# Kernel tuning notes

Measured on AMD Instinct MI355X. Metric: run time of the kernel, lower is better.

The kernel has to match this reference:

```python
import jax, jax.numpy as jnp
import numpy as np

B, S, D, H = 8, 2048, 768, 12

def setup_inputs() -> dict:
    key = jax.random.key(0)
    kx, km, kk, kq, kv = jax.random.split(key, 5)
    return {
        "x": jax.random.normal(kx, (B, S, D), dtype=jnp.float32),
        "mask": jax.random.randint(km, (B, 1, S), 0, 2, dtype=jnp.int32),
        "key_weight": jax.random.normal(kk, (D, H), dtype=jnp.float32),
        "query_weight": jax.random.normal(kq, (D, H), dtype=jnp.float32),
        "value_weight": jax.random.normal(kv, (D, H), dtype=jnp.float32),
    }

def reference(x, mask, key_weight, query_weight, value_weight):
    scale = 1.0 / (key_weight.shape[-1] ** 0.5)
    k = jnp.einsum('bsd,dh->bsh', x, key_weight)
    q = jnp.einsum('bsd,dh->bsh', x, query_weight)
    v = jnp.einsum('bsd,dh->bsh', x, value_weight)
    # scores: (B, S, T) — full score matrix as in the original
    scores = jnp.einsum('bsh,bth->bst', q, k) * scale
    scores = jnp.where(mask == 0, -jnp.inf, scores)
    attn = jax.nn.softmax(scores, axis=-1)
    return jnp.einsum('bst,bth->bsh', attn, v)
```

## Files before the change

### kernel.cpp

```cpp
#include <hip/hip_runtime.h>
#include <math.h>

#define QSCALE (0.2886751345948129f * 1.4426950408889634f)

#if __has_builtin(__builtin_amdgcn_exp2f)
#define EXP2F(x) __builtin_amdgcn_exp2f(x)
#else
#define EXP2F(x) exp2f(x)
#endif

typedef __attribute__((ext_vector_type(8))) _Float16 half8;
typedef __attribute__((ext_vector_type(4))) _Float16 half4_t;
typedef __attribute__((ext_vector_type(4))) float floatx4;

#define MFMA32F16(a, b, c) __builtin_amdgcn_mfma_f32_16x16x32_f16((a), (b), (c), 0, 0, 0)
#define MFMA16F16(a, b, c) __builtin_amdgcn_mfma_f32_16x16x16f16((a), (b), (c), 0, 0, 0)

static __device__ inline float bperm(float v, int addr_bytes) {
    return __int_as_float(__builtin_amdgcn_ds_bpermute(addr_bytes, __float_as_int(v)));
}

__global__ __launch_bounds__(256)
void wswz(const float* __restrict__ Wq, const float* __restrict__ Wk,
          const float* __restrict__ Wv, _Float16* __restrict__ wfh,
          _Float16* __restrict__ wfl)
{
    int t = blockIdx.x * 256 + threadIdx.x;
    if (t >= 4608) return;
    int lane = t & 63;
    int nt   = (t >> 6) % 3;
    int ks   = t / 192;
    const float* W = (nt == 0) ? Wq : (nt == 1) ? Wk : Wv;
    const float scale = (nt == 0) ? QSCALE : 1.0f;
    int col = lane & 15;
    int q8  = lane >> 4;
    half8 hi, lo;
    #pragma unroll
    for (int j = 0; j < 8; ++j) {
        int dim = ks * 32 + q8 * 8 + j;
        float f = (col < 12) ? W[dim * 12 + col] * scale : 0.0f;
        _Float16 h = (_Float16)f;
        hi[j] = h;
        lo[j] = (_Float16)(f - (float)h);
    }
    size_t off = ((size_t)(ks * 3 + nt) * 64 + lane) * 8;
    *(half8*)(wfh + off) = hi;
    *(half8*)(wfl + off) = lo;
}

__global__ __launch_bounds__(256)
void mask_scan(const int* __restrict__ mask, int* __restrict__ dst,
               int* __restrict__ nvalid)
{
    __shared__ int cnt[256];
    const int b = blockIdx.x;
    const int t = threadIdx.x;
    const int* mb = mask + b * 2048;
    int local[8]; int c = 0;
    #pragma unroll
    for (int i = 0; i < 8; ++i) { local[i] = (mb[t * 8 + i] != 0); c += local[i]; }
    cnt[t] = c;
    __syncthreads();
    for (int off = 1; off < 256; off <<= 1) {
        int u = cnt[t];
        int add = (t >= off) ? cnt[t - off] : 0;
        __syncthreads();
        cnt[t] = u + add;
        __syncthreads();
    }
    int run = (t == 0) ? 0 : cnt[t - 1];
    int* db = dst + b * 2048;
    #pragma unroll
    for (int i = 0; i < 8; ++i) { db[t * 8 + i] = local[i] ? run : -1; run += local[i]; }
    if (t == 255) nvalid[b] = cnt[255];
}

__global__ __launch_bounds__(256)
void zero_frag(float4* __restrict__ p, int n)
{
    int i = blockIdx.x * 256 + threadIdx.x;
    float4 z = make_float4(0.f, 0.f, 0.f, 0.f);
    if (i < n) p[i] = z;
}

__global__ __launch_bounds__(256, 2)
void qkv_mfma(const float* __restrict__ x, const _Float16* __restrict__ wfh,
              const _Float16* __restrict__ wfl, const int* __restrict__ dst,
              _Float16* __restrict__ qfh, _Float16* __restrict__ qfl,
              _Float16* __restrict__ kfh, _Float16* __restrict__ kfl,
              _Float16* __restrict__ vtf)
{
    __shared__ float xs[12352];
    const int tid  = threadIdx.x;
    const int lane = tid & 63;
    const int w    = tid >> 6;
    const int g    = blockIdx.x;
    const int rowbase = g * 16;

    {
        const int r  = tid >> 4;
        const int c0 = (tid & 15) * 4;
        const float* xr = x + (size_t)(rowbase + r) * 768 + c0;
        float* xd = xs + r * 772 + c0;
        #pragma unroll
        for (int i = 0; i < 12; ++i) {
            float4 v = *(const float4*)(xr + i * 64);
            *(float4*)(xd + i * 64) = v;
        }
    }
    __syncthreads();

    floatx4 acc0 = {0.f, 0.f, 0.f, 0.f};
    floatx4 acc1 = acc0, acc2 = acc0;
    const int m15 = lane & 15;
    const int q8  = lane >> 4;
    const float* xsrc = xs + m15 * 772 + q8 * 8;
    const half8* WH = (const half8*)wfh;
    const half8* WL = (const half8*)wfl;

    #pragma unroll
    for (int s6 = 0; s6 < 6; ++s6) {
        const int ks = w * 6 + s6;
        float xv[8];
        *(float4*)(xv)     = *(const float4*)(xsrc + ks * 32);
        *(float4*)(xv + 4) = *(const float4*)(xsrc + ks * 32 + 4);
        half8 ah, al;
        #pragma unroll
        for (int j = 0; j < 8; ++j) {
            _Float16 h = (_Float16)xv[j];
            ah[j] = h;
            al[j] = (_Float16)(xv[j] - (float)h);
        }
        half8 b0h = WH[(ks * 3 + 0) * 64 + lane];
        half8 b1h = WH[(ks * 3 + 1) * 64 + lane];
        half8 b2h = WH[(ks * 3 + 2) * 64 + lane];
        half8 b0l = WL[(ks * 3 + 0) * 64 + lane];
        half8 b1l = WL[(ks * 3 + 1) * 64 + lane];
        half8 b2l = WL[(ks * 3 + 2) * 64 + lane];
        acc0 = MFMA32F16(ah, b0h, acc0);
        acc1 = MFMA32F16(ah, b1h, acc1);
        acc2 = MFMA32F16(ah, b2h, acc2);
        acc0 = MFMA32F16(al, b0h, acc0);
        acc1 = MFMA32F16(al, b1h, acc1);
        acc2 = MFMA32F16(al, b2h, acc2);
        acc0 = MFMA32F16(ah, b0l, acc0);
        acc1 = MFMA32F16(ah, b1l, acc1);
        acc2 = MFMA32F16(ah, b2l, acc2);
    }

    __syncthreads();
    float* cbuf = xs;
    *(floatx4*)(cbuf + ((w * 3 + 0) * 64 + lane) * 4) = acc0;
    *(floatx4*)(cbuf + ((w * 3 + 1) * 64 + lane) * 4) = acc1;
    *(floatx4*)(cbuf + ((w * 3 + 2) * 64 + lane) * 4) = acc2;
    __syncthreads();
    if (w < 3) {
        floatx4 t0 = *(const floatx4*)(cbuf + ((0 * 3 + w) * 64 + lane) * 4);
        floatx4 t1 = *(const floatx4*)(cbuf + ((1 * 3 + w) * 64 + lane) * 4);
        floatx4 t2 = *(const floatx4*)(cbuf + ((2 * 3 + w) * 64 + lane) * 4);
        floatx4 t3 = *(const floatx4*)(cbuf + ((3 * 3 + w) * 64 + lane) * 4);
        floatx4 tot = t0 + t1 + t2 + t3;
        const int col = m15;
        const int r0  = q8 * 4;
        #pragma unroll
        for (int r = 0; r < 4; ++r) {
            const int row = rowbase + r0 + r;
            const float val = tot[r];
            if (w == 0) {
                if (col < 12) {
                    size_t off = ((size_t)g * 64 + (col >> 3) * 16 + (r0 + r)) * 8 + (col & 7);
                    _Float16 h = (_Float16)val;
                    qfh[off] = h;
                    qfl[off] = (_Float16)(val - (float)h);
                }
            } else {
                const int d = dst[row];
                if (d >= 0) {
                    const int bb = row >> 11;
                    if (w == 1) {
                        if (col < 12) {
                            size_t off = (((size_t)(bb * 128 + (d >> 4))) * 64
                                          + (col >> 3) * 16 + (d & 15)) * 8 + (col & 7);
                            _Float16 h = (_Float16)val;
                            kfh[off] = h;
                            kfl[off] = (_Float16)(val - (float)h);
                        }
                    } else {
                        if (col < 12) {
                            size_t off = (((size_t)(bb * 128 + (d >> 4))) * 64
                                          + ((d & 15) >> 2) * 16 + col) * 4 + (d & 3);
                            vtf[off] = (_Float16)val;
                        } else if (col == 12) {
                            size_t off = (((size_t)(bb * 128 + (d >> 4))) * 64
                                          + ((d & 15) >> 2) * 16 + 12) * 4 + (d & 3);
                            vtf[off] = (_Float16)1.0f;
                        }
                    }
                }
            }
        }
    }
}

__global__ __launch_bounds__(256)
void attn(const _Float16* __restrict__ qfh, const _Float16* __restrict__ qfl,
          const _Float16* __restrict__ kfh, const _Float16* __restrict__ kfl,
          const _Float16* __restrict__ vtf, const int* __restrict__ nvalid,
          float* __restrict__ out)
{
    __shared__ float cm[256];
    __shared__ __align__(16) floatx4 co[256];
    const int tid  = threadIdx.x;
    const int lane = tid & 63;
    const int w    = tid >> 6;
    const int g    = blockIdx.x;
    const int bb   = g >> 7;
    const int m15  = lane & 15;

    const half8 qh = *(const half8*)(qfh + ((size_t)g * 64 + lane) * 8);
    const half8 ql = *(const half8*)(qfl + ((size_t)g * 64 + lane) * 8);

    const half8* KH = (const half8*)kfh + (size_t)bb * 128 * 64;
    const half8* KL = (const half8*)kfl + (size_t)bb * 128 * 64;
    const half4_t* VT = (const half4_t*)vtf + (size_t)bb * 128 * 64;

    const int nv = nvalid[bb];
    const int nt = (nv + 15) >> 4;
    const int a16 = (lane ^ 16) << 2;
    const int a32 = (lane ^ 32) << 2;

    float mrow = -INFINITY;
    floatx4 o = {0.f, 0.f, 0.f, 0.f};

    int t = w;
    half8 kh, kl;
    half4_t va;
    if (t < nt) {
        kh = KH[t * 64 + lane];
        kl = KL[t * 64 + lane];
        va = VT[t * 64 + lane];
    }
    for (; t < nt; t += 4) {
        half8 nkh, nkl; half4_t nva;
        if (t + 4 < nt) {
            nkh = KH[(t + 4) * 64 + lane];
            nkl = KL[(t + 4) * 64 + lane];
            nva = VT[(t + 4) * 64 + lane];
        }
        floatx4 s = {0.f, 0.f, 0.f, 0.f};
        s = MFMA32F16(kh, qh, s);
        s = MFMA32F16(kl, qh, s);
        s = MFMA32F16(kh, ql, s);
        float pm = fmaxf(fmaxf(s.x, s.y), fmaxf(s.z, s.w));
        pm = fmaxf(pm, bperm(pm, a16));
        pm = fmaxf(pm, bperm(pm, a32));
        float mnew = fmaxf(mrow, pm);
        float corr = EXP2F(mrow - mnew);
        o.x *= corr; o.y *= corr; o.z *= corr; o.w *= corr;
        half4_t pb;
        pb[0] = (_Float16)EXP2F(s.x - mnew);
        pb[1] = (_Float16)EXP2F(s.y - mnew);
        pb[2] = (_Float16)EXP2F(s.z - mnew);
        pb[3] = (_Float16)EXP2F(s.w - mnew);
        o = MFMA16F16(va, pb, o);
        mrow = mnew;
        kh = nkh; kl = nkl; va = nva;
    }

    cm[w * 64 + lane] = mrow;
    co[w * 64 + lane] = o;
    __syncthreads();
    float gm = -INFINITY;
    #pragma unroll
    for (int w2 = 0; w2 < 4; ++w2) gm = fmaxf(gm, cm[w2 * 64 + lane]);
    floatx4 O = {0.f, 0.f, 0.f, 0.f};
    #pragma unroll
    for (int w2 = 0; w2 < 4; ++w2) {
        float f = EXP2F(cm[w2 * 64 + lane] - gm);
        floatx4 ow = co[w2 * 64 + lane];
        O.x += ow.x * f; O.y += ow.y * f; O.z += ow.z * f; O.w += ow.w * f;
    }
    float L = bperm(O.x, (48 + m15) << 2);
    float inv = 1.0f / L;
    if (w == 0 && (lane >> 4) < 3) {
        float4 ov = make_float4(O.x * inv, O.y * inv, O.z * inv, O.w * inv);
        *(float4*)(out + ((size_t)g * 16 + m15) * 12 + (lane >> 4) * 4) = ov;
    }
}

extern "C" void kernel_launch(void* const* d_in, const int* in_sizes, int n_in,
                              void* d_out, int out_size, void* d_ws, size_t ws_size,
                              hipStream_t stream) {
    const float* x    = (const float*)d_in[0];
    const int*   mask = (const int*)  d_in[1];
    const float* Wk   = (const float*)d_in[2];
    const float* Wq   = (const float*)d_in[3];
    const float* Wv   = (const float*)d_in[4];
    float* out = (float*)d_out;

    char* base = (char*)d_ws;
    _Float16* qfh = (_Float16*)(base);
    _Float16* qfl = (_Float16*)(base + (1u << 20));
    _Float16* kfh = (_Float16*)(base + (2u << 20));
    _Float16* kfl = (_Float16*)(base + (3u << 20));
    _Float16* vtf = (_Float16*)(base + (4u << 20));
    _Float16* wfh = (_Float16*)(base + 4718592);
    _Float16* wfl = (_Float16*)(base + 4718592 + 73728);
    int* dst      = (int*)(base + 4866048);
    int* nvalid   = (int*)(base + 4866048 + 65536);

    const int zero_n = 4718592 / 16;
    wswz<<<18, 256, 0, stream>>>(Wq, Wk, Wv, wfh, wfl);
    mask_scan<<<8, 256, 0, stream>>>(mask, dst, nvalid);
    zero_frag<<<(zero_n + 255) / 256, 256, 0, stream>>>((float4*)base, zero_n);
    qkv_mfma<<<1024, 256, 0, stream>>>(x, wfh, wfl, dst, qfh, qfl, kfh, kfl, vtf);
    attn<<<1024, 256, 0, stream>>>(qfh, qfl, kfh, kfl, vtf, nvalid, out);
}
```

Measured before the change: 115.2 us.

## Fuse prep kernels, load x directly in QKV, and process two query tiles per attention block

Merges the weight swizzle, mask scan and fragment zeroing into one prep launch, and zeroes only the K/V fragment region. The QKV kernel reads x straight from global memory into registers instead of staging it in LDS, prefetches weight fragments with double buffering, and targets higher occupancy. The attention kernel handles two 16-row query tiles per block, so each K/V fragment load feeds two score/PV computations, and blocks are interleaved across batches. Register pressure rises in both kernels, and the reduced zeroing range assumes the Q buffers are fully overwritten.

```diff
diff --git a/kernel.cpp b/kernel.cpp
--- a/kernel.cpp
+++ b/kernel.cpp
@@ -21,135 +21,133 @@
 }
 
 __global__ __launch_bounds__(256)
-void wswz(const float* __restrict__ Wq, const float* __restrict__ Wk,
-          const float* __restrict__ Wv, _Float16* __restrict__ wfh,
-          _Float16* __restrict__ wfl)
+void prep(const float* __restrict__ Wq, const float* __restrict__ Wk,
+          const float* __restrict__ Wv, const int* __restrict__ mask,
+          _Float16* __restrict__ wfh, _Float16* __restrict__ wfl,
+          int* __restrict__ dst, int* __restrict__ nvalid,
+          float4* __restrict__ zbase)
 {
-    int t = blockIdx.x * 256 + threadIdx.x;
-    if (t >= 4608) return;
-    int lane = t & 63;
-    int nt   = (t >> 6) % 3;
-    int ks   = t / 192;
-    const float* W = (nt == 0) ? Wq : (nt == 1) ? Wk : Wv;
-    const float scale = (nt == 0) ? QSCALE : 1.0f;
-    int col = lane & 15;
-    int q8  = lane >> 4;
-    half8 hi, lo;
-    #pragma unroll
-    for (int j = 0; j < 8; ++j) {
-        int dim = ks * 32 + q8 * 8 + j;
-        float f = (col < 12) ? W[dim * 12 + col] * scale : 0.0f;
-        _Float16 h = (_Float16)f;
-        hi[j] = h;
-        lo[j] = (_Float16)(f - (float)h);
-    }
-    size_t off = ((size_t)(ks * 3 + nt) * 64 + lane) * 8;
-    *(half8*)(wfh + off) = hi;
-    *(half8*)(wfl + off) = lo;
-}
-
-__global__ __launch_bounds__(256)
-void mask_scan(const int* __restrict__ mask, int* __restrict__ dst,
-               int* __restrict__ nvalid)
-{
-    __shared__ int cnt[256];
     const int b = blockIdx.x;
-    const int t = threadIdx.x;
-    const int* mb = mask + b * 2048;
-    int local[8]; int c = 0;
-    #pragma unroll
-    for (int i = 0; i < 8; ++i) { local[i] = (mb[t * 8 + i] != 0); c += local[i]; }
-    cnt[t] = c;
-    __syncthreads();
-    for (int off = 1; off < 256; off <<= 1) {
-        int u = cnt[t];
-        int add = (t >= off) ? cnt[t - off] : 0;
+    const int tid = threadIdx.x;
+    if (b < 18) {
+        int t = b * 256 + tid;
+        if (t >= 4608) return;
+        int lane = t & 63;
+        int nt   = (t >> 6) % 3;
+        int ks   = t / 192;
+        const float* W = (nt == 0) ? Wq : (nt == 1) ? Wk : Wv;
+        const float scale = (nt == 0) ? QSCALE : 1.0f;
+        int col = lane & 15;
+        int q8  = lane >> 4;
+        half8 hi, lo;
+        #pragma unroll
+        for (int j = 0; j < 8; ++j) {
+            int dim = ks * 32 + q8 * 8 + j;
+            float f = (col < 12) ? W[dim * 12 + col] * scale : 0.0f;
+            _Float16 h = (_Float16)f;
+            hi[j] = h;
+            lo[j] = (_Float16)(f - (float)h);
+        }
+        size_t off = ((size_t)(ks * 3 + nt) * 64 + lane) * 8;
+        *(half8*)(wfh + off) = hi;
+        *(half8*)(wfl + off) = lo;
+    } else if (b < 26) {
+        __shared__ int cnt[256];
+        const int bb = b - 18;
+        const int* mb = mask + bb * 2048;
+        int local[8]; int c = 0;
+        #pragma unroll
+        for (int i = 0; i < 8; ++i) { local[i] = (mb[tid * 8 + i] != 0); c += local[i]; }
+        cnt[tid] = c;
         __syncthreads();
-        cnt[t] = u + add;
-        __syncthreads();
-    }
-    int run = (t == 0) ? 0 : cnt[t - 1];
-    int* db = dst + b * 2048;
-    #pragma unroll
-    for (int i = 0; i < 8; ++i) { db[t * 8 + i] = local[i] ? run : -1; run += local[i]; }
-    if (t == 255) nvalid[b] = cnt[255];
-}
-
-__global__ __launch_bounds__(256)
-void zero_frag(float4* __restrict__ p, int n)
-{
-    int i = blockIdx.x * 256 + threadIdx.x;
-    float4 z = make_float4(0.f, 0.f, 0.f, 0.f);
-    if (i < n) p[i] = z;
-}
-
-__global__ __launch_bounds__(256, 2)
+        for (int off = 1; off < 256; off <<= 1) {
+            int u = cnt[tid];
+            int add = (tid >= off) ? cnt[tid - off] : 0;
+            __syncthreads();
+            cnt[tid] = u + add;
+            __syncthreads();
+        }
+        int run = (tid == 0) ? 0 : cnt[tid - 1];
+        int* db = dst + bb * 2048;
+        #pragma unroll
+        for (int i = 0; i < 8; ++i) { db[tid * 8 + i] = local[i] ? run : -1; run += local[i]; }
+        if (tid == 255) nvalid[bb] = cnt[255];
+    } else {
+        const float4 z = make_float4(0.f, 0.f, 0.f, 0.f);
+        for (int i = (b - 26) * 256 + tid; i < 163840; i += 6 * 256) zbase[i] = z;
+    }
+}
+
+__global__ __launch_bounds__(256, 3)
 void qkv_mfma(const float* __restrict__ x, const _Float16* __restrict__ wfh,
               const _Float16* __restrict__ wfl, const int* __restrict__ dst,
               _Float16* __restrict__ qfh, _Float16* __restrict__ qfl,
               _Float16* __restrict__ kfh, _Float16* __restrict__ kfl,
               _Float16* __restrict__ vtf)
 {
-    __shared__ float xs[12352];
+    __shared__ __align__(16) float cbuf[3072];
     const int tid  = threadIdx.x;
     const int lane = tid & 63;
     const int w    = tid >> 6;
     const int g    = blockIdx.x;
     const int rowbase = g * 16;
-
-    {
-        const int r  = tid >> 4;
-        const int c0 = (tid & 15) * 4;
-        const float* xr = x + (size_t)(rowbase + r) * 768 + c0;
-        float* xd = xs + r * 772 + c0;
-        #pragma unroll
-        for (int i = 0; i < 12; ++i) {
-            float4 v = *(const float4*)(xr + i * 64);
-            *(float4*)(xd + i * 64) = v;
-        }
-    }
-    __syncthreads();
+    const int m15 = lane & 15;
+    const int q8  = lane >> 4;
+
+    const float* xbase = x + (size_t)(rowbase + m15) * 768 + q8 * 8;
+    const half8* WH = (const half8*)wfh;
+    const half8* WL = (const half8*)wfl;
+
+    float xv[6][8];
+    #pragma unroll
+    for (int s = 0; s < 6; ++s) {
+        const int ks = w * 6 + s;
+        *(float4*)(xv[s])     = *(const float4*)(xbase + ks * 32);
+        *(float4*)(xv[s] + 4) = *(const float4*)(xbase + ks * 32 + 4);
+    }
 
     floatx4 acc0 = {0.f, 0.f, 0.f, 0.f};
     floatx4 acc1 = acc0, acc2 = acc0;
-    const int m15 = lane & 15;
-    const int q8  = lane >> 4;
-    const float* xsrc = xs + m15 * 772 + q8 * 8;
-    const half8* WH = (const half8*)wfh;
-    const half8* WL = (const half8*)wfl;
+
+    half8 bh[2][3], bl[2][3];
+    {
+        const int ks = w * 6;
+        #pragma unroll
+        for (int n = 0; n < 3; ++n) {
+            bh[0][n] = WH[(ks * 3 + n) * 64 + lane];
+            bl[0][n] = WL[(ks * 3 + n) * 64 + lane];
+        }
+    }
 
     #pragma unroll
-    for (int s6 = 0; s6 < 6; ++s6) {
-        const int ks = w * 6 + s6;
-        float xv[8];
-        *(float4*)(xv)     = *(const float4*)(xsrc + ks * 32);
-        *(float4*)(xv + 4) = *(const float4*)(xsrc + ks * 32 + 4);
+    for (int s = 0; s < 6; ++s) {
+        const int cur = s & 1, nxt = cur ^ 1;
+        if (s < 5) {
+            const int ksn = w * 6 + s + 1;
+            #pragma unroll
+            for (int n = 0; n < 3; ++n) {
+                bh[nxt][n] = WH[(ksn * 3 + n) * 64 + lane];
+                bl[nxt][n] = WL[(ksn * 3 + n) * 64 + lane];
+            }
+        }
         half8 ah, al;
         #pragma unroll
         for (int j = 0; j < 8; ++j) {
-            _Float16 h = (_Float16)xv[j];
+            _Float16 h = (_Float16)xv[s][j];
             ah[j] = h;
-            al[j] = (_Float16)(xv[j] - (float)h);
-        }
-        half8 b0h = WH[(ks * 3 + 0) * 64 + lane];
-        half8 b1h = WH[(ks * 3 + 1) * 64 + lane];
-        half8 b2h = WH[(ks * 3 + 2) * 64 + lane];
-        half8 b0l = WL[(ks * 3 + 0) * 64 + lane];
-        half8 b1l = WL[(ks * 3 + 1) * 64 + lane];
-        half8 b2l = WL[(ks * 3 + 2) * 64 + lane];
-        acc0 = MFMA32F16(ah, b0h, acc0);
-        acc1 = MFMA32F16(ah, b1h, acc1);
-        acc2 = MFMA32F16(ah, b2h, acc2);
-        acc0 = MFMA32F16(al, b0h, acc0);
-        acc1 = MFMA32F16(al, b1h, acc1);
-        acc2 = MFMA32F16(al, b2h, acc2);
-        acc0 = MFMA32F16(ah, b0l, acc0);
-        acc1 = MFMA32F16(ah, b1l, acc1);
-        acc2 = MFMA32F16(ah, b2l, acc2);
-    }
-
-    __syncthreads();
-    float* cbuf = xs;
+            al[j] = (_Float16)(xv[s][j] - (float)h);
+        }
+        acc0 = MFMA32F16(ah, bh[cur][0], acc0);
+        acc1 = MFMA32F16(ah, bh[cur][1], acc1);
+        acc2 = MFMA32F16(ah, bh[cur][2], acc2);
+        acc0 = MFMA32F16(al, bh[cur][0], acc0);
+        acc1 = MFMA32F16(al, bh[cur][1], acc1);
+        acc2 = MFMA32F16(al, bh[cur][2], acc2);
+        acc0 = MFMA32F16(ah, bl[cur][0], acc0);
+        acc1 = MFMA32F16(ah, bl[cur][1], acc1);
+        acc2 = MFMA32F16(ah, bl[cur][2], acc2);
+    }
+
     *(floatx4*)(cbuf + ((w * 3 + 0) * 64 + lane) * 4) = acc0;
     *(floatx4*)(cbuf + ((w * 3 + 1) * 64 + lane) * 4) = acc1;
     *(floatx4*)(cbuf + ((w * 3 + 2) * 64 + lane) * 4) = acc2;
@@ -208,17 +206,20 @@
           const _Float16* __restrict__ vtf, const int* __restrict__ nvalid,
           float* __restrict__ out)
 {
-    __shared__ float cm[256];
-    __shared__ __align__(16) floatx4 co[256];
+    __shared__ float cm[512];
+    __shared__ __align__(16) floatx4 co[512];
     const int tid  = threadIdx.x;
     const int lane = tid & 63;
     const int w    = tid >> 6;
-    const int g    = blockIdx.x;
-    const int bb   = g >> 7;
+    const int bb   = blockIdx.x & 7;
+    const int gl   = blockIdx.x >> 3;
+    const int g0   = bb * 128 + gl * 2;
     const int m15  = lane & 15;
 
-    const half8 qh = *(const half8*)(qfh + ((size_t)g * 64 + lane) * 8);
-    const half8 ql = *(const half8*)(qfl + ((size_t)g * 64 + lane) * 8);
+    const half8 qh0 = *(const half8*)(qfh + ((size_t)g0 * 64 + lane) * 8);
+    const half8 ql0 = *(const half8*)(qfl + ((size_t)g0 * 64 + lane) * 8);
+    const half8 qh1 = *(const half8*)(qfh + ((size_t)(g0 + 1) * 64 + lane) * 8);
+    const half8 ql1 = *(const half8*)(qfl + ((size_t)(g0 + 1) * 64 + lane) * 8);
 
     const half8* KH = (const half8*)kfh + (size_t)bb * 128 * 64;
     const half8* KL = (const half8*)kfl + (size_t)bb * 128 * 64;
@@ -229,8 +230,9 @@
     const int a16 = (lane ^ 16) << 2;
     const int a32 = (lane ^ 32) << 2;
 
-    float mrow = -INFINITY;
-    floatx4 o = {0.f, 0.f, 0.f, 0.f};
+    float m0 = -INFINITY, m1 = -INFINITY;
+    floatx4 o0 = {0.f, 0.f, 0.f, 0.f};
+    floatx4 o1 = o0;
 
     int t = w;
     half8 kh, kl;
@@ -247,44 +249,70 @@
             nkl = KL[(t + 4) * 64 + lane];
             nva = VT[(t + 4) * 64 + lane];
         }
-        floatx4 s = {0.f, 0.f, 0.f, 0.f};
-        s = MFMA32F16(kh, qh, s);
-        s = MFMA32F16(kl, qh, s);
-        s = MFMA32F16(kh, ql, s);
-        float pm = fmaxf(fmaxf(s.x, s.y), fmaxf(s.z, s.w));
-        pm = fmaxf(pm, bperm(pm, a16));
-        pm = fmaxf(pm, bperm(pm, a32));
-        float mnew = fmaxf(mrow, pm);
-        float corr = EXP2F(mrow - mnew);
-        o.x *= corr; o.y *= corr; o.z *= corr; o.w *= corr;
-        half4_t pb;
-        pb[0] = (_Float16)EXP2F(s.x - mnew);
-        pb[1] = (_Float16)EXP2F(s.y - mnew);
-        pb[2] = (_Float16)EXP2F(s.z - mnew);
-        pb[3] = (_Float16)EXP2F(s.w - mnew);
-        o = MFMA16F16(va, pb, o);
-        mrow = mnew;
+        floatx4 s0 = {0.f, 0.f, 0.f, 0.f};
+        floatx4 s1 = s0;
+        s0 = MFMA32F16(kh, qh0, s0);
+        s1 = MFMA32F16(kh, qh1, s1);
+        s0 = MFMA32F16(kl, qh0, s0);
+        s1 = MFMA32F16(kl, qh1, s1);
+        s0 = MFMA32F16(kh, ql0, s0);
+        s1 = MFMA32F16(kh, ql1, s1);
+        {
+            float pm = fmaxf(fmaxf(s0.x, s0.y), fmaxf(s0.z, s0.w));
+            pm = fmaxf(pm, bperm(pm, a16));
+            pm = fmaxf(pm, bperm(pm, a32));
+            float mnew = fmaxf(m0, pm);
+            float corr = EXP2F(m0 - mnew);
+            o0.x *= corr; o0.y *= corr; o0.z *= corr; o0.w *= corr;
+            half4_t pb;
+            pb[0] = (_Float16)EXP2F(s0.x - mnew);
+            pb[1] = (_Float16)EXP2F(s0.y - mnew);
+            pb[2] = (_Float16)EXP2F(s0.z - mnew);
+            pb[3] = (_Float16)EXP2F(s0.w - mnew);
+            o0 = MFMA16F16(va, pb, o0);
+            m0 = mnew;
+        }
+        {
+            float pm = fmaxf(fmaxf(s1.x, s1.y), fmaxf(s1.z, s1.w));
+            pm = fmaxf(pm, bperm(pm, a16));
+            pm = fmaxf(pm, bperm(pm, a32));
+            float mnew = fmaxf(m1, pm);
+            float corr = EXP2F(m1 - mnew);
+            o1.x *= corr; o1.y *= corr; o1.z *= corr; o1.w *= corr;
+            half4_t pb;
+            pb[0] = (_Float16)EXP2F(s1.x - mnew);
+            pb[1] = (_Float16)EXP2F(s1.y - mnew);
+            pb[2] = (_Float16)EXP2F(s1.z - mnew);
+            pb[3] = (_Float16)EXP2F(s1.w - mnew);
+            o1 = MFMA16F16(va, pb, o1);
+            m1 = mnew;
+        }
         kh = nkh; kl = nkl; va = nva;
     }
 
-    cm[w * 64 + lane] = mrow;
-    co[w * 64 + lane] = o;
+    cm[(0 * 4 + w) * 64 + lane] = m0;
+    cm[(1 * 4 + w) * 64 + lane] = m1;
+    co[(0 * 4 + w) * 64 + lane] = o0;
+    co[(1 * 4 + w) * 64 + lane] = o1;
     __syncthreads();
-    float gm = -INFINITY;
-    #pragma unroll
-    for (int w2 = 0; w2 < 4; ++w2) gm = fmaxf(gm, cm[w2 * 64 + lane]);
-    floatx4 O = {0.f, 0.f, 0.f, 0.f};
-    #pragma unroll
-    for (int w2 = 0; w2 < 4; ++w2) {
-        float f = EXP2F(cm[w2 * 64 + lane] - gm);
-        floatx4 ow = co[w2 * 64 + lane];
-        O.x += ow.x * f; O.y += ow.y * f; O.z += ow.z * f; O.w += ow.w * f;
-    }
-    float L = bperm(O.x, (48 + m15) << 2);
-    float inv = 1.0f / L;
-    if (w == 0 && (lane >> 4) < 3) {
-        float4 ov = make_float4(O.x * inv, O.y * inv, O.z * inv, O.w * inv);
-        *(float4*)(out + ((size_t)g * 16 + m15) * 12 + (lane >> 4) * 4) = ov;
+    if (w < 2) {
+        const int gi = w;
+        float gm = -INFINITY;
+        #pragma unroll
+        for (int w2 = 0; w2 < 4; ++w2) gm = fmaxf(gm, cm[(gi * 4 + w2) * 64 + lane]);
+        floatx4 O = {0.f, 0.f, 0.f, 0.f};
+        #pragma unroll
+        for (int w2 = 0; w2 < 4; ++w2) {
+            float f = EXP2F(cm[(gi * 4 + w2) * 64 + lane] - gm);
+            floatx4 ow = co[(gi * 4 + w2) * 64 + lane];
+            O.x += ow.x * f; O.y += ow.y * f; O.z += ow.z * f; O.w += ow.w * f;
+        }
+        float L = bperm(O.x, (48 + m15) << 2);
+        float inv = 1.0f / L;
+        if ((lane >> 4) < 3) {
+            float4 ov = make_float4(O.x * inv, O.y * inv, O.z * inv, O.w * inv);
+            *(float4*)(out + ((size_t)(g0 + gi) * 16 + m15) * 12 + (lane >> 4) * 4) = ov;
+        }
     }
 }
 
@@ -308,11 +336,9 @@
     _Float16* wfl = (_Float16*)(base + 4718592 + 73728);
     int* dst      = (int*)(base + 4866048);
     int* nvalid   = (int*)(base + 4866048 + 65536);
-
-    const int zero_n = 4718592 / 16;
-    wswz<<<18, 256, 0, stream>>>(Wq, Wk, Wv, wfh, wfl);
-    mask_scan<<<8, 256, 0, stream>>>(mask, dst, nvalid);
-    zero_frag<<<(zero_n + 255) / 256, 256, 0, stream>>>((float4*)base, zero_n);
+    float4* zbase = (float4*)(base + (2u << 20));
+
+    prep<<<32, 256, 0, stream>>>(Wq, Wk, Wv, mask, wfh, wfl, dst, nvalid, zbase);
     qkv_mfma<<<1024, 256, 0, stream>>>(x, wfh, wfl, dst, qfh, qfl, kfh, kfl, vtf);
-    attn<<<1024, 256, 0, stream>>>(qfh, qfl, kfh, kfl, vtf, nvalid, out);
-}
+    attn<<<512, 256, 0, stream>>>(qfh, qfl, kfh, kfl, vtf, nvalid, out);
+}
```

Result: no change. 113.3 us (-1.6%).
